# Performance work log

Hardware: AMD Instinct MI355X
Metric: run time of the kernel (lower is better)

## Reference

```python
import jax, jax.numpy as jnp
import numpy as np

N = 4096
D = 512   # d_model == dff (required by the original code path)
H = 4
NEG = -1e10
ALPHA = 0.3  # keras LeakyReLU default alpha


def setup_inputs() -> dict:
    key = jax.random.key(0)
    ks = jax.random.split(key, 8)
    nodes = jax.random.normal(ks[0], (N, D), dtype=jnp.float32)
    # sparse-ish 0/1 dense adjacency with self loops
    adj = (jax.random.uniform(ks[1], (N, N)) < 0.01).astype(jnp.float32)
    adj = jnp.maximum(adj, jnp.eye(N, dtype=jnp.float32))
    s = 0.05
    W_node = jax.random.normal(ks[2], (D, D), dtype=jnp.float32) * s
    b_node = jnp.zeros((D,), dtype=jnp.float32)
    K = jax.random.normal(ks[3], (H, D, D), dtype=jnp.float32) * s
    A_self = jax.random.normal(ks[4], (H, D), dtype=jnp.float32) * s
    A_neigh = jax.random.normal(ks[5], (H, D), dtype=jnp.float32) * s
    return {"nodes": nodes, "adj": adj, "W_node": W_node, "b_node": b_node,
            "K": K, "A_self": A_self, "A_neigh": A_neigh, "num_heads": H}


def reference(nodes, adj, W_node, b_node, K, A_self, A_neigh, num_heads):
    # node_layer: Dense(dff)
    x = nodes @ W_node + b_node                       # [N, D]
    # per-head projection, vectorized over heads
    feats = jnp.einsum('nd,hdf->hnf', x, K)           # [H, N, D]
    # additive attention scores; both terms are per-row scalars -> [H, N]
    s = jnp.einsum('hnf,hf->hn', feats, A_self) + jnp.einsum('hnf,hf->hn', feats, A_neigh)
    s = jnp.where(s > 0, s, ALPHA * s)                # LeakyReLU(alpha=0.3)
    # broadcast row score over columns + adjacency mask, softmax over neighbors
    logits = s[:, :, None] + NEG * (1.0 - adj)[None]  # [H, N, N]
    attn = jax.nn.softmax(logits, axis=-1)
    # dropout is identity at inference (training=False)
    out = jnp.einsum('hij,hjf->hif', attn, feats)     # [H, N, D]
    out = jnp.mean(out, axis=0)                       # mean over heads
    return jax.nn.relu(out)
```

## Files before the change

### kernel.cpp

```cpp
#include <hip/hip_runtime.h>
#include <hip/hip_bf16.h>


typedef short  short8 __attribute__((ext_vector_type(8)));
typedef float  f32x4  __attribute__((ext_vector_type(4)));

__device__ inline unsigned short f2bf(float f) {
    union { float f; unsigned int u; } v; v.f = f;
    unsigned int u = v.u;
    u += 0x7fffu + ((u >> 16) & 1u);
    return (unsigned short)(u >> 16);
}

__global__ void kbarT_kernel(const float* __restrict__ K, unsigned short* __restrict__ KbarT,
                             int D, int H, float invH) {
    int idx = blockIdx.x * 256 + threadIdx.x;
    int DD = D * D;
    if (idx >= DD) return;
    int f = idx / D, d = idx - f * D;
    float s = 0.f;
    for (int h = 0; h < H; ++h) s += K[(size_t)h * DD + d * D + f];
    KbarT[idx] = f2bf(s * invH);
}

__global__ void cast_bf16_kernel(const float* __restrict__ in, unsigned short* __restrict__ out,
                                 int n8) {
    int idx = blockIdx.x * 256 + threadIdx.x;
    if (idx >= n8) return;
    const float4* p = reinterpret_cast<const float4*>(in) + (size_t)idx * 2;
    float4 a = p[0], b = p[1];
    short8 v;
    v[0] = (short)f2bf(a.x); v[1] = (short)f2bf(a.y);
    v[2] = (short)f2bf(a.z); v[3] = (short)f2bf(a.w);
    v[4] = (short)f2bf(b.x); v[5] = (short)f2bf(b.y);
    v[6] = (short)f2bf(b.z); v[7] = (short)f2bf(b.w);
    *reinterpret_cast<short8*>(out + (size_t)idx * 8) = v;
}

__global__ __launch_bounds__(256) void bias2_kernel(
        const float* __restrict__ b, const unsigned short* __restrict__ KbarT,
        float* __restrict__ bias2, int D) {
    int wid  = (blockIdx.x * 256 + threadIdx.x) >> 6;
    int lane = threadIdx.x & 63;
    if (wid >= D) return;
    const unsigned short* kr = KbarT + (size_t)wid * D + lane * 8;
    const float* br = b + lane * 8;
    float s = 0.f;
#pragma unroll
    for (int j = 0; j < 8; ++j) {
        union { unsigned int i; float f; } v; v.i = ((unsigned int)kr[j]) << 16;
        s += br[j] * v.f;
    }
#pragma unroll
    for (int off = 32; off; off >>= 1) s += __shfl_down(s, off, 64);
    if (lane == 0) bias2[wid] = s;
}

__global__ __launch_bounds__(256) void gemm_bf16_kernel(
        const unsigned short* __restrict__ A,
        const unsigned short* __restrict__ Bt,
        const float* __restrict__ bias,
        unsigned short* __restrict__ C,
        int M, int Nn, int K) {
    __shared__ unsigned short As[64][32];
    __shared__ unsigned short Bs[64][32];
    const int tid  = threadIdx.x;
    const int lane = tid & 63;
    const int wave = tid >> 6;
    const int wy = wave >> 1, wx = wave & 1;
    const int row0 = blockIdx.y * 64, col0 = blockIdx.x * 64;
    const int l15 = lane & 15, quad = lane >> 4;

    const int ldr = tid >> 2;
    const int ldk = (tid & 3) * 8;

    f32x4 acc[2][2] = {};

    for (int k0 = 0; k0 < K; k0 += 32) {
        short8 av = *reinterpret_cast<const short8*>(&A [(size_t)(row0 + ldr) * K + k0 + ldk]);
        short8 bv = *reinterpret_cast<const short8*>(&Bt[(size_t)(col0 + ldr) * K + k0 + ldk]);
        __syncthreads();
        *reinterpret_cast<short8*>(&As[ldr][ldk]) = av;
        *reinterpret_cast<short8*>(&Bs[ldr][ldk]) = bv;
        __syncthreads();
        short8 a0 = *reinterpret_cast<const short8*>(&As[wy * 32 +      l15][quad * 8]);
        short8 a1 = *reinterpret_cast<const short8*>(&As[wy * 32 + 16 + l15][quad * 8]);
        short8 b0 = *reinterpret_cast<const short8*>(&Bs[wx * 32 +      l15][quad * 8]);
        short8 b1 = *reinterpret_cast<const short8*>(&Bs[wx * 32 + 16 + l15][quad * 8]);
        acc[0][0] = __builtin_amdgcn_mfma_f32_16x16x32_bf16(a0, b0, acc[0][0], 0, 0, 0);
        acc[0][1] = __builtin_amdgcn_mfma_f32_16x16x32_bf16(a0, b1, acc[0][1], 0, 0, 0);
        acc[1][0] = __builtin_amdgcn_mfma_f32_16x16x32_bf16(a1, b0, acc[1][0], 0, 0, 0);
        acc[1][1] = __builtin_amdgcn_mfma_f32_16x16x32_bf16(a1, b1, acc[1][1], 0, 0, 0);
    }

#pragma unroll
    for (int mi = 0; mi < 2; ++mi)
#pragma unroll
        for (int ni = 0; ni < 2; ++ni) {
            int col = col0 + wx * 32 + ni * 16 + l15;
            float bv = bias ? bias[col] : 0.f;
#pragma unroll
            for (int r = 0; r < 4; ++r) {
                int row = row0 + wy * 32 + mi * 16 + quad * 4 + r;
                C[(size_t)row * Nn + col] = f2bf(acc[mi][ni][r] + bv);
            }
        }
}

__global__ __launch_bounds__(256) void aggregate_kernel(
        const float* __restrict__ adj, const unsigned short* __restrict__ g,
        float* __restrict__ out, int N, int D) {
    const int row = blockIdx.x;
    const int tid = threadIdx.x;
    __shared__ int lst[1024];
    __shared__ int cnt;
    if (tid == 0) cnt = 0;
    __syncthreads();

    const float* arow = adj + (size_t)row * N;
    const int nper = N >> 8;
    const int base = tid * nper;
    const float4* ap = reinterpret_cast<const float4*>(arow + base);
    for (int c = 0; c < (nper >> 2); ++c) {
        float4 a = ap[c];
        int b4 = base + c * 4;
        if (a.x > 0.5f) { int p = atomicAdd(&cnt, 1); if (p < 1024) lst[p] = b4;     }
        if (a.y > 0.5f) { int p = atomicAdd(&cnt, 1); if (p < 1024) lst[p] = b4 + 1; }
        if (a.z > 0.5f) { int p = atomicAdd(&cnt, 1); if (p < 1024) lst[p] = b4 + 2; }
        if (a.w > 0.5f) { int p = atomicAdd(&cnt, 1); if (p < 1024) lst[p] = b4 + 3; }
    }
    __syncthreads();
    int deg = cnt; if (deg > 1024) deg = 1024;

    const int col = tid * 2;
    float acc0 = 0.f, acc1 = 0.f;
    int k = 0;
    for (; k + 8 <= deg; k += 8) {
        unsigned int u[8];
#pragma unroll
        for (int j = 0; j < 8; ++j)
            u[j] = *reinterpret_cast<const unsigned int*>(&g[(size_t)lst[k + j] * D + col]);
#pragma unroll
        for (int j = 0; j < 8; ++j) {
            union { unsigned int i; float f; } lo, hi;
            lo.i = u[j] << 16; hi.i = u[j] & 0xffff0000u;
            acc0 += lo.f; acc1 += hi.f;
        }
    }
    for (; k < deg; ++k) {
        unsigned int u = *reinterpret_cast<const unsigned int*>(&g[(size_t)lst[k] * D + col]);
        union { unsigned int i; float f; } lo, hi;
        lo.i = u << 16; hi.i = u & 0xffff0000u;
        acc0 += lo.f; acc1 += hi.f;
    }

    float inv = deg > 0 ? 1.f / (float)deg : 0.f;
    acc0 *= inv; acc1 *= inv;
    float2 o;
    o.x = acc0 > 0.f ? acc0 : 0.f;
    o.y = acc1 > 0.f ? acc1 : 0.f;
    *reinterpret_cast<float2*>(&out[(size_t)row * D + col]) = o;
}

extern "C" void kernel_launch(void* const* d_in, const int* in_sizes, int n_in,
                              void* d_out, int out_size, void* d_ws, size_t ws_size,
                              hipStream_t stream) {
    const float* nodes  = (const float*)d_in[0];
    const float* adj    = (const float*)d_in[1];
    const float* W_node = (const float*)d_in[2];
    const float* b_node = (const float*)d_in[3];
    const float* K      = (const float*)d_in[4];

    const int D  = in_sizes[3];
    const int N  = in_sizes[0] / D;
    const int H  = in_sizes[4] / (D * D);
    const int DD = D * D;

    float* out = (float*)d_out;

    char* ws = (char*)d_ws;
    unsigned short* KbarT    = (unsigned short*)(ws);
    unsigned short* W_bf16   = (unsigned short*)(ws + (size_t)DD * 2);
    unsigned short* MmatT    = (unsigned short*)(ws + (size_t)DD * 4);
    unsigned short* nodes_bf = (unsigned short*)(ws + (size_t)DD * 6);
    unsigned short* g_bf16   = (unsigned short*)(ws + (size_t)DD * 6 + (size_t)N * D * 2);
    float*          bias2    = (float*)        (ws + (size_t)DD * 6 + (size_t)N * D * 4);

    kbarT_kernel<<<(DD + 255) / 256, 256, 0, stream>>>(K, KbarT, D, H, 1.0f / (float)H);

    cast_bf16_kernel<<<(DD / 8 + 255) / 256, 256, 0, stream>>>(W_node, W_bf16, DD / 8);
    cast_bf16_kernel<<<(N * D / 8 + 255) / 256, 256, 0, stream>>>(nodes, nodes_bf, N * D / 8);

    bias2_kernel<<<(D * 64 + 255) / 256, 256, 0, stream>>>(b_node, KbarT, bias2, D);

    {
        dim3 grid(D / 64, D / 64);
        gemm_bf16_kernel<<<grid, 256, 0, stream>>>(KbarT, W_bf16, nullptr, MmatT, D, D, D);
    }

    {
        dim3 grid(D / 64, N / 64);
        gemm_bf16_kernel<<<grid, 256, 0, stream>>>(nodes_bf, MmatT, bias2, g_bf16, N, D, D);
    }

    aggregate_kernel<<<N, 256, 0, stream>>>(adj, g_bf16, out, N, D);
}
```

Baseline: 162.0 us.

## Fuse bf16 casts into GEMM loads, tile K-bar transpose, merge bias kernel

Removes the separate fp32-to-bf16 cast kernels for nodes and W_node; the GEMMs now read fp32 and convert while staging tiles into shared memory. The per-head K averaging and transpose now go through a 64x64 shared-memory tile, so both global reads and writes are coalesced instead of strided. The bias2 reduction runs as extra blocks of the first GEMM launch. Together this cuts the launch count and the intermediate bf16 buffer traffic. The cost is that GEMM2 reads fp32 nodes with twice the bytes per tile load.

After: 159.9 us. Within noise of the previous version (-1.3%).

```diff
diff --git a/kernel.cpp b/kernel.cpp
--- a/kernel.cpp
+++ b/kernel.cpp
@@ -1,5 +1,4 @@
 #include <hip/hip_runtime.h>
-#include <hip/hip_bf16.h>
 
 
 typedef short  short8 __attribute__((ext_vector_type(8)));
@@ -12,73 +11,83 @@
     return (unsigned short)(u >> 16);
 }
 
-__global__ void kbarT_kernel(const float* __restrict__ K, unsigned short* __restrict__ KbarT,
-                             int D, int H, float invH) {
-    int idx = blockIdx.x * 256 + threadIdx.x;
-    int DD = D * D;
-    if (idx >= DD) return;
-    int f = idx / D, d = idx - f * D;
-    float s = 0.f;
-    for (int h = 0; h < H; ++h) s += K[(size_t)h * DD + d * D + f];
-    KbarT[idx] = f2bf(s * invH);
-}
-
-__global__ void cast_bf16_kernel(const float* __restrict__ in, unsigned short* __restrict__ out,
-                                 int n8) {
-    int idx = blockIdx.x * 256 + threadIdx.x;
-    if (idx >= n8) return;
-    const float4* p = reinterpret_cast<const float4*>(in) + (size_t)idx * 2;
-    float4 a = p[0], b = p[1];
-    short8 v;
-    v[0] = (short)f2bf(a.x); v[1] = (short)f2bf(a.y);
-    v[2] = (short)f2bf(a.z); v[3] = (short)f2bf(a.w);
-    v[4] = (short)f2bf(b.x); v[5] = (short)f2bf(b.y);
-    v[6] = (short)f2bf(b.z); v[7] = (short)f2bf(b.w);
-    *reinterpret_cast<short8*>(out + (size_t)idx * 8) = v;
-}
-
-__global__ __launch_bounds__(256) void bias2_kernel(
-        const float* __restrict__ b, const unsigned short* __restrict__ KbarT,
-        float* __restrict__ bias2, int D) {
-    int wid  = (blockIdx.x * 256 + threadIdx.x) >> 6;
-    int lane = threadIdx.x & 63;
-    if (wid >= D) return;
-    const unsigned short* kr = KbarT + (size_t)wid * D + lane * 8;
-    const float* br = b + lane * 8;
-    float s = 0.f;
-#pragma unroll
-    for (int j = 0; j < 8; ++j) {
-        union { unsigned int i; float f; } v; v.i = ((unsigned int)kr[j]) << 16;
-        s += br[j] * v.f;
-    }
-#pragma unroll
-    for (int off = 32; off; off >>= 1) s += __shfl_down(s, off, 64);
-    if (lane == 0) bias2[wid] = s;
-}
-
-__global__ __launch_bounds__(256) void gemm_bf16_kernel(
-        const unsigned short* __restrict__ A,
-        const unsigned short* __restrict__ Bt,
-        const float* __restrict__ bias,
-        unsigned short* __restrict__ C,
-        int M, int Nn, int K) {
+__global__ __launch_bounds__(256) void kbarT_kernel(
+        const float* __restrict__ K, unsigned short* __restrict__ KbarT,
+        int D, int H, float invH) {
+    __shared__ float tile[64][65];
+    const int f0 = blockIdx.x * 64, d0 = blockIdx.y * 64;
+    const int tid = threadIdx.x;
+    const int c4 = (tid & 15) * 4;
+    const int DD = D * D;
+
+    for (int rr = tid >> 4; rr < 64; rr += 16) {
+        float sx = 0.f, sy = 0.f, sz = 0.f, sw = 0.f;
+        for (int h = 0; h < H; ++h) {
+            float4 v = *reinterpret_cast<const float4*>(
+                &K[(size_t)h * DD + (size_t)(d0 + rr) * D + f0 + c4]);
+            sx += v.x; sy += v.y; sz += v.z; sw += v.w;
+        }
+        tile[rr][c4 + 0] = sx * invH;
+        tile[rr][c4 + 1] = sy * invH;
+        tile[rr][c4 + 2] = sz * invH;
+        tile[rr][c4 + 3] = sw * invH;
+    }
+    __syncthreads();
+    for (int fr = tid >> 4; fr < 64; fr += 16) {
+        ushort4 o;
+        o.x = f2bf(tile[c4 + 0][fr]);
+        o.y = f2bf(tile[c4 + 1][fr]);
+        o.z = f2bf(tile[c4 + 2][fr]);
+        o.w = f2bf(tile[c4 + 3][fr]);
+        *reinterpret_cast<ushort4*>(&KbarT[(size_t)(f0 + fr) * D + d0 + c4]) = o;
+    }
+}
+
+template <bool CA, bool CB>
+__device__ inline void gemm_body(const void* __restrict__ Ap,
+                                 const void* __restrict__ Btp,
+                                 const float* __restrict__ bias,
+                                 unsigned short* __restrict__ C,
+                                 int Nn, int K, int bx, int by) {
     __shared__ unsigned short As[64][32];
     __shared__ unsigned short Bs[64][32];
     const int tid  = threadIdx.x;
     const int lane = tid & 63;
     const int wave = tid >> 6;
     const int wy = wave >> 1, wx = wave & 1;
-    const int row0 = blockIdx.y * 64, col0 = blockIdx.x * 64;
+    const int row0 = by * 64, col0 = bx * 64;
     const int l15 = lane & 15, quad = lane >> 4;
-
     const int ldr = tid >> 2;
     const int ldk = (tid & 3) * 8;
 
     f32x4 acc[2][2] = {};
 
     for (int k0 = 0; k0 < K; k0 += 32) {
-        short8 av = *reinterpret_cast<const short8*>(&A [(size_t)(row0 + ldr) * K + k0 + ldk]);
-        short8 bv = *reinterpret_cast<const short8*>(&Bt[(size_t)(col0 + ldr) * K + k0 + ldk]);
+        short8 av, bv;
+        if (CA) {
+            const float* a = (const float*)Ap + (size_t)(row0 + ldr) * K + k0 + ldk;
+            float4 x = *reinterpret_cast<const float4*>(a);
+            float4 y = *reinterpret_cast<const float4*>(a + 4);
+            av[0] = (short)f2bf(x.x); av[1] = (short)f2bf(x.y);
+            av[2] = (short)f2bf(x.z); av[3] = (short)f2bf(x.w);
+            av[4] = (short)f2bf(y.x); av[5] = (short)f2bf(y.y);
+            av[6] = (short)f2bf(y.z); av[7] = (short)f2bf(y.w);
+        } else {
+            av = *reinterpret_cast<const short8*>(
+                (const unsigned short*)Ap + (size_t)(row0 + ldr) * K + k0 + ldk);
+        }
+        if (CB) {
+            const float* b = (const float*)Btp + (size_t)(col0 + ldr) * K + k0 + ldk;
+            float4 x = *reinterpret_cast<const float4*>(b);
+            float4 y = *reinterpret_cast<const float4*>(b + 4);
+            bv[0] = (short)f2bf(x.x); bv[1] = (short)f2bf(x.y);
+            bv[2] = (short)f2bf(x.z); bv[3] = (short)f2bf(x.w);
+            bv[4] = (short)f2bf(y.x); bv[5] = (short)f2bf(y.y);
+            bv[6] = (short)f2bf(y.z); bv[7] = (short)f2bf(y.w);
+        } else {
+            bv = *reinterpret_cast<const short8*>(
+                (const unsigned short*)Btp + (size_t)(col0 + ldr) * K + k0 + ldk);
+        }
         __syncthreads();
         *reinterpret_cast<short8*>(&As[ldr][ldk]) = av;
         *reinterpret_cast<short8*>(&Bs[ldr][ldk]) = bv;
@@ -98,13 +107,45 @@
 #pragma unroll
         for (int ni = 0; ni < 2; ++ni) {
             int col = col0 + wx * 32 + ni * 16 + l15;
-            float bv = bias ? bias[col] : 0.f;
+            float bvl = bias ? bias[col] : 0.f;
 #pragma unroll
             for (int r = 0; r < 4; ++r) {
                 int row = row0 + wy * 32 + mi * 16 + quad * 4 + r;
-                C[(size_t)row * Nn + col] = f2bf(acc[mi][ni][r] + bv);
+                C[(size_t)row * Nn + col] = f2bf(acc[mi][ni][r] + bvl);
             }
         }
+}
+
+__global__ __launch_bounds__(256) void gemm1_kernel(
+        const unsigned short* __restrict__ KbarT, const float* __restrict__ W,
+        const float* __restrict__ b, unsigned short* __restrict__ MmatT,
+        float* __restrict__ bias2, int D, int gemmY) {
+    if ((int)blockIdx.y >= gemmY) {
+        int e = ((int)blockIdx.y - gemmY) * gridDim.x + blockIdx.x;
+        int wave = threadIdx.x >> 6, lane = threadIdx.x & 63;
+        int f = e * 4 + wave;
+        if (f >= D) return;
+        const unsigned short* kr = KbarT + (size_t)f * D + lane * 8;
+        const float* br = b + lane * 8;
+        float s = 0.f;
+#pragma unroll
+        for (int j = 0; j < 8; ++j) {
+            union { unsigned int i; float f; } v; v.i = ((unsigned int)kr[j]) << 16;
+            s += br[j] * v.f;
+        }
+#pragma unroll
+        for (int off = 32; off; off >>= 1) s += __shfl_down(s, off, 64);
+        if (lane == 0) bias2[f] = s;
+        return;
+    }
+    gemm_body<false, true>(KbarT, W, nullptr, MmatT, D, D, blockIdx.x, blockIdx.y);
+}
+
+__global__ __launch_bounds__(256) void gemm2_kernel(
+        const float* __restrict__ nodes, const unsigned short* __restrict__ MmatT,
+        const float* __restrict__ bias2, unsigned short* __restrict__ g,
+        int D, int K) {
+    gemm_body<true, false>(nodes, MmatT, bias2, g, D, K, blockIdx.x, blockIdx.y);
 }
 
 __global__ __launch_bounds__(256) void aggregate_kernel(
@@ -179,28 +220,26 @@
     float* out = (float*)d_out;
 
     char* ws = (char*)d_ws;
-    unsigned short* KbarT    = (unsigned short*)(ws);
-    unsigned short* W_bf16   = (unsigned short*)(ws + (size_t)DD * 2);
-    unsigned short* MmatT    = (unsigned short*)(ws + (size_t)DD * 4);
-    unsigned short* nodes_bf = (unsigned short*)(ws + (size_t)DD * 6);
-    unsigned short* g_bf16   = (unsigned short*)(ws + (size_t)DD * 6 + (size_t)N * D * 2);
-    float*          bias2    = (float*)        (ws + (size_t)DD * 6 + (size_t)N * D * 4);
-
-    kbarT_kernel<<<(DD + 255) / 256, 256, 0, stream>>>(K, KbarT, D, H, 1.0f / (float)H);
-
-    cast_bf16_kernel<<<(DD / 8 + 255) / 256, 256, 0, stream>>>(W_node, W_bf16, DD / 8);
-    cast_bf16_kernel<<<(N * D / 8 + 255) / 256, 256, 0, stream>>>(nodes, nodes_bf, N * D / 8);
-
-    bias2_kernel<<<(D * 64 + 255) / 256, 256, 0, stream>>>(b_node, KbarT, bias2, D);
+    unsigned short* KbarT  = (unsigned short*)(ws);
+    unsigned short* MmatT  = (unsigned short*)(ws + (size_t)DD * 2);
+    unsigned short* g_bf16 = (unsigned short*)(ws + (size_t)DD * 4);
+    float*          bias2  = (float*)        (ws + (size_t)DD * 4 + (size_t)N * D * 2);
 
     {
         dim3 grid(D / 64, D / 64);
-        gemm_bf16_kernel<<<grid, 256, 0, stream>>>(KbarT, W_bf16, nullptr, MmatT, D, D, D);
+        kbarT_kernel<<<grid, 256, 0, stream>>>(K, KbarT, D, H, 1.0f / (float)H);
+    }
+
+    {
+        int gx = D / 64, gemmY = D / 64;
+        int biasRows = (D / 4 + gx - 1) / gx;
+        dim3 grid(gx, gemmY + biasRows);
+        gemm1_kernel<<<grid, 256, 0, stream>>>(KbarT, W_node, b_node, MmatT, bias2, D, gemmY);
     }
 
     {
         dim3 grid(D / 64, N / 64);
-        gemm_bf16_kernel<<<grid, 256, 0, stream>>>(nodes_bf, MmatT, bias2, g_bf16, N, D, D);
+        gemm2_kernel<<<grid, 256, 0, stream>>>(nodes, MmatT, bias2, g_bf16, D, D);
     }
 
     aggregate_kernel<<<N, 256, 0, stream>>>(adj, g_bf16, out, N, D);
```
